# Kernel tuning notes

Measured on AMD Instinct MI355X. Metric: run time of the kernel, lower is better.

## Reference

```python
import jax, jax.numpy as jnp
import numpy as np

C = 64          # channels
K = 15          # sum(shell_sizes)=1+14
H = 32          # neighbors per query
N = 50000       # support points (== query points M)
RADIUS = 1.0
SIGMA = 0.7
INF = 1e6
BN_EPS = 1e-5


def _init_kernel_points(key):
    # stand-in for load_kernels: 1 center point + 14 points on a sphere shell
    pts = jax.random.normal(key, (K - 1, 3), dtype=jnp.float32)
    pts = pts / jnp.linalg.norm(pts, axis=1, keepdims=True) * RADIUS
    return jnp.concatenate([jnp.zeros((1, 3), jnp.float32), pts], axis=0)


def setup_inputs() -> dict:
    key = jax.random.key(0)
    ks = jax.random.split(key, 10)
    q_pts = jax.random.normal(ks[0], (N, 3), dtype=jnp.float32)
    s_pts = jax.random.normal(ks[1], (N, 3), dtype=jnp.float32)
    s_feats = jax.random.normal(ks[2], (N, C), dtype=jnp.float32)
    neighb_inds = jax.random.randint(ks[3], (N, H), 0, N)
    kernel_points = _init_kernel_points(ks[4])
    # alpha_mlp: Linear(C->C, no bias) -> BatchNorm -> LeakyReLU(0.1) -> Linear(C->K*C)
    lim1 = 1.0 / np.sqrt(C)
    W1 = jax.random.uniform(ks[5], (C, C), jnp.float32, -lim1, lim1)
    gamma = jnp.ones((C,), jnp.float32)
    beta = jnp.zeros((C,), jnp.float32)
    W2 = jax.random.uniform(ks[6], (C, K * C), jnp.float32, -lim1, lim1)
    b2 = jax.random.uniform(ks[7], (K * C,), jnp.float32, -lim1, lim1)
    return {"q_pts": q_pts, "s_pts": s_pts, "s_feats": s_feats,
            "neighb_inds": neighb_inds, "kernel_points": kernel_points,
            "W1": W1, "gamma": gamma, "beta": beta, "W2": W2, "b2": b2}


def reference(q_pts, s_pts, s_feats, neighb_inds, kernel_points, W1, gamma, beta, W2, b2):
    M = q_pts.shape[0]
    # alpha_mlp on pooled (= center) features: (M, C) -> (M, K*C)
    h = s_feats @ W1
    mu = jnp.mean(h, axis=0)
    var = jnp.var(h, axis=0)
    h = (h - mu) / jnp.sqrt(var + BN_EPS) * gamma + beta
    h = jax.nn.leaky_relu(h, 0.1)
    conv_weights = (h @ W2 + b2).reshape(M, K, C)

    # gather neighbor features with a zero padding row (index N -> zeros)
    padded_feats = jnp.concatenate([s_feats, jnp.zeros((1, C), s_feats.dtype)], axis=0)
    neighbor_feats = padded_feats[neighb_inds]                 # (M, H, C)

    # relative neighbor positions with inf padding point
    s_pts_pad = jnp.concatenate([s_pts, jnp.full((1, 3), INF, s_pts.dtype)], axis=0)
    neighbors = s_pts_pad[neighb_inds] - q_pts[:, None, :]     # (M, H, 3)

    # kernel-point influence: nearest kernel point + linear influence
    diff = neighbors[:, :, None, :] - kernel_points            # (M, H, K, 3)
    sq_d = jnp.sum(diff * diff, axis=-1)                       # (M, H, K)
    nn_sq = jnp.min(sq_d, axis=-1)                             # (M, H)
    nn_idx = jnp.argmin(sq_d, axis=-1)                         # (M, H)
    infl = jnp.clip(1.0 - jnp.sqrt(nn_sq) / SIGMA, 0.0)        # (M, H)

    # per-neighbor channel weights from the MLP output, gathered by 1nn kernel point
    nw = jnp.take_along_axis(conv_weights, nn_idx[:, :, None], axis=1)  # (M, H, C)
    nw = nw * infl[:, :, None]

    # weighted aggregation (merge=mul, aggr=sum over neighbors)
    return jnp.sum(neighbor_feats * nw, axis=1)                # (M, C)
```

## Files before the change

kernel.cpp:

```cpp
#include <hip/hip_runtime.h>
#include <math.h>

#define N_PTS 50000
#define CCH   64
#define KP    15
#define NH    32
#define SIGMA 0.7f
#define BN_EPS 1e-5f
#define LEAKY 0.1f
#define QB    16
#define STATS_BLOCKS 1024
#define SP4_BLOCKS 196
#define CW_KSTRIDE_B 2176

typedef short bf16x8 __attribute__((ext_vector_type(8)));
typedef float floatx4 __attribute__((ext_vector_type(4)));

__device__ __forceinline__ unsigned short f2b(float f) {
    union { float f; unsigned u; } v; v.f = f;
    return (unsigned short)((v.u + 0x7FFFu + ((v.u >> 16) & 1u)) >> 16);
}
__device__ __forceinline__ float b2f(unsigned short b) {
    union { unsigned u; float f; } v; v.u = ((unsigned)b) << 16;
    return v.f;
}
__device__ __forceinline__ float blo(unsigned u) {
    union { unsigned u; float f; } v; v.u = u << 16;
    return v.f;
}
__device__ __forceinline__ float bhi(unsigned u) {
    union { unsigned u; float f; } v; v.u = u & 0xFFFF0000u;
    return v.f;
}
__device__ __forceinline__ unsigned cvtpk(float lo, float hi) {
    unsigned r;
    asm("v_cvt_pk_bf16_f32 %0, %1, %2" : "=v"(r) : "v"(lo), "v"(hi));
    return r;
}

__global__ __launch_bounds__(256) void k_prep(const float* __restrict__ sf,
                                              const float* __restrict__ W1,
                                              const float* __restrict__ W2,
                                              const float* __restrict__ s_pts,
                                              float* __restrict__ bn,
                                              unsigned short* __restrict__ hst,
                                              unsigned short* __restrict__ w2b,
                                              unsigned short* __restrict__ sfb,
                                              float* __restrict__ sp4) {
    int t = threadIdx.x;
    if (blockIdx.x >= STATS_BLOCKS + 30) {
        int g = (blockIdx.x - STATS_BLOCKS - 30) * 256 + t;
        if (g < N_PTS) {
            float4 v;
            v.x = s_pts[g * 3 + 0]; v.y = s_pts[g * 3 + 1];
            v.z = s_pts[g * 3 + 2]; v.w = 0.f;
            *(float4*)(sp4 + g * 4) = v;
        }
        return;
    }
    if (blockIdx.x >= STATS_BLOCKS) {
        int g = (blockIdx.x - STATS_BLOCKS) * 256 + t;
        int lane = g & 63, s = (g >> 6) & 1, tt = g >> 7;
        int col = lane & 15, quad = lane >> 4;
        int base = (s * 32 + quad * 8) * 960 + tt * 16 + col;
        ushort4 lo, hi;
        lo.x = f2b(W2[base + 0 * 960]); lo.y = f2b(W2[base + 1 * 960]);
        lo.z = f2b(W2[base + 2 * 960]); lo.w = f2b(W2[base + 3 * 960]);
        hi.x = f2b(W2[base + 4 * 960]); hi.y = f2b(W2[base + 5 * 960]);
        hi.z = f2b(W2[base + 6 * 960]); hi.w = f2b(W2[base + 7 * 960]);
        *(ushort4*)(w2b + g * 8)     = lo;
        *(ushort4*)(w2b + g * 8 + 4) = hi;
        return;
    }
    int c = t & 63, ml = t >> 6;
    float w1c[64];
    #pragma unroll
    for (int i = 0; i < 64; ++i) w1c[i] = W1[i * 64 + c];
    __shared__ float rows[4][64];
    float acc_s = 0.f, acc_q = 0.f;
    for (int m0 = blockIdx.x * 4; m0 < N_PTS; m0 += STATS_BLOCKS * 4) {
        __syncthreads();
        float v = sf[m0 * 64 + t];
        ((float*)rows)[t] = v;
        sfb[m0 * 64 + t] = f2b(v);
        __syncthreads();
        float h = 0.f;
        #pragma unroll
        for (int i4 = 0; i4 < 16; ++i4) {
            float4 r = *(const float4*)&rows[ml][i4 * 4];
            h += r.x * w1c[i4 * 4] + r.y * w1c[i4 * 4 + 1]
               + r.z * w1c[i4 * 4 + 2] + r.w * w1c[i4 * 4 + 3];
        }
        acc_s += h;
        acc_q += h * h;
        hst[(m0 + ml) * 64 + c] = f2b(h);
    }
    __shared__ float red[2][256];
    red[0][t] = acc_s; red[1][t] = acc_q;
    __syncthreads();
    if (t < 64) {
        float s = red[0][t] + red[0][64 + t] + red[0][128 + t] + red[0][192 + t];
        float q = red[1][t] + red[1][64 + t] + red[1][128 + t] + red[1][192 + t];
        atomicAdd(&bn[t], s);
        atomicAdd(&bn[64 + t], q);
    }
}

__global__ __launch_bounds__(256, 4) void k_main(
    const float* __restrict__ q_pts, const float* __restrict__ sp4,
    const unsigned short* __restrict__ sfb, const int* __restrict__ nb,
    const float* __restrict__ kpts, const float* __restrict__ gamma,
    const float* __restrict__ beta, const float* __restrict__ bn,
    const float* __restrict__ b2, const unsigned short* __restrict__ w2b,
    const unsigned short* __restrict__ hst, float* __restrict__ out) {

    __shared__ __align__(16) unsigned cwP[KP * 32 * 17];
    __shared__ float abS[128];
    __shared__ int      nCnt[QB];
    __shared__ unsigned nPack[QB][NH];
    __shared__ float    nInf[QB][NH];

    int t = threadIdx.x;
    int lane = t & 63, wv = t >> 6;
    int m0 = blockIdx.x * QB;

    int q0 = t >> 5, hh = t & 31;
    int q1 = q0 + 8;
    int idx0 = nb[(m0 + q0) * NH + hh];
    int idx1 = nb[(m0 + q1) * NH + hh];

    if (t < 64) {
        float mu  = bn[t] * (1.0f / N_PTS);
        float var = bn[64 + t] * (1.0f / N_PTS) - mu * mu;
        float a   = gamma[t] * rsqrtf(var + BN_EPS);
        abS[t]      = a;
        abS[64 + t] = beta[t] - mu * a;
    }
    ((unsigned*)nPack)[t]       = 0u;
    ((unsigned*)nPack)[t + 256] = 0u;
    ((float*)nInf)[t]           = 0.f;
    ((float*)nInf)[t + 256]     = 0.f;

    int row = lane & 15, half = lane >> 4;
    bf16x8 r0, r1;
    {
        const unsigned short* hrow = hst + (m0 + row) * 64 + half * 8;
        r0 = *(const bf16x8*)(hrow);
        r1 = *(const bf16x8*)(hrow + 32);
    }

    float4 sp0 = *(const float4*)(sp4 + idx0 * 4);
    float4 sp1 = *(const float4*)(sp4 + idx1 * 4);
    float qx0 = q_pts[(m0 + q0) * 3 + 0], qy0 = q_pts[(m0 + q0) * 3 + 1],
          qz0 = q_pts[(m0 + q0) * 3 + 2];
    float qx1 = q_pts[(m0 + q1) * 3 + 0], qy1 = q_pts[(m0 + q1) * 3 + 1],
          qz1 = q_pts[(m0 + q1) * 3 + 2];

    float kpr[45];
    #pragma unroll
    for (int i = 0; i < 45; ++i) kpr[i] = kpts[i];

    __syncthreads();

    unsigned pf0 = 0, pf1 = 0, pf2 = 0, pf3 = 0;
    {
        float px = sp0.x - qx0, py = sp0.y - qy0, pz = sp0.z - qz0;
        float best = 1e30f; int bi = 0;
        #pragma unroll
        for (int k = 0; k < KP; ++k) {
            float dx = px - kpr[k * 3], dy = py - kpr[k * 3 + 1], dz = pz - kpr[k * 3 + 2];
            float d = dx * dx + dy * dy + dz * dz;
            if (d < best) { best = d; bi = k; }
        }
        float infl = 1.f - sqrtf(best) * (1.0f / SIGMA);
        bool keep = infl > 0.f;
        unsigned long long bal = __ballot(keep);
        unsigned mym = (unsigned)(bal >> (lane & 32));
        int pos = __popc(mym & ((1u << (lane & 31)) - 1u));
        if (keep) {
            nPack[q0][pos] = (unsigned)idx0 | ((unsigned)(bi * CW_KSTRIDE_B) << 16);
            nInf[q0][pos]  = infl;
            const unsigned* rowp = (const unsigned*)(sfb + idx0 * 64);
            pf0 = rowp[0]; pf1 = rowp[16];
        }
        if ((lane & 31) == 0) nCnt[q0] = __popc(mym);
    }
    {
        float px = sp1.x - qx1, py = sp1.y - qy1, pz = sp1.z - qz1;
        float best = 1e30f; int bi = 0;
        #pragma unroll
        for (int k = 0; k < KP; ++k) {
            float dx = px - kpr[k * 3], dy = py - kpr[k * 3 + 1], dz = pz - kpr[k * 3 + 2];
            float d = dx * dx + dy * dy + dz * dz;
            if (d < best) { best = d; bi = k; }
        }
        float infl = 1.f - sqrtf(best) * (1.0f / SIGMA);
        bool keep = infl > 0.f;
        unsigned long long bal = __ballot(keep);
        unsigned mym = (unsigned)(bal >> (lane & 32));
        int pos = __popc(mym & ((1u << (lane & 31)) - 1u));
        if (keep) {
            nPack[q1][pos] = (unsigned)idx1 | ((unsigned)(bi * CW_KSTRIDE_B) << 16);
            nInf[q1][pos]  = infl;
            const unsigned* rowp = (const unsigned*)(sfb + idx1 * 64);
            pf2 = rowp[0]; pf3 = rowp[16];
        }
        if ((lane & 31) == 0) nCnt[q1] = __popc(mym);
    }

    bf16x8 a0, a1;
    {
        unsigned* A0 = (unsigned*)&a0;
        unsigned* A1 = (unsigned*)&a1;
        #pragma unroll
        for (int jw = 0; jw < 4; ++jw) {
            int c0 = half * 8 + jw * 2;
            float g00 = abS[c0]     * b2f((unsigned short)r0[jw * 2])     + abS[64 + c0];
            float g01 = abS[c0 + 1] * b2f((unsigned short)r0[jw * 2 + 1]) + abS[64 + c0 + 1];
            g00 = g00 > 0.f ? g00 : LEAKY * g00;
            g01 = g01 > 0.f ? g01 : LEAKY * g01;
            A0[jw] = cvtpk(g00, g01);
            int c1 = 32 + c0;
            float g10 = abS[c1]     * b2f((unsigned short)r1[jw * 2])     + abS[64 + c1];
            float g11 = abS[c1 + 1] * b2f((unsigned short)r1[jw * 2 + 1]) + abS[64 + c1 + 1];
            g10 = g10 > 0.f ? g10 : LEAKY * g10;
            g11 = g11 > 0.f ? g11 : LEAKY * g11;
            A1[jw] = cvtpk(g10, g11);
        }
    }

    {
        int colq = lane & 15, quad = lane >> 4;
        bf16x8 Lf[3], Ls[3], Mf[3], Ms[3];
        #pragma unroll
        for (int i = 0; i < 3; ++i) {
            int tt = wv * 15 + i;
            Lf[i] = *(const bf16x8*)(w2b + ((tt * 2 + 0) * 64 + lane) * 8);
            Ls[i] = *(const bf16x8*)(w2b + ((tt * 2 + 1) * 64 + lane) * 8);
        }
        #pragma unroll
        for (int g = 0; g < 5; ++g) {
            if (g < 4) {
                #pragma unroll
                for (int i = 0; i < 3; ++i) {
                    int tt = wv * 15 + (g + 1) * 3 + i;
                    Mf[i] = *(const bf16x8*)(w2b + ((tt * 2 + 0) * 64 + lane) * 8);
                    Ms[i] = *(const bf16x8*)(w2b + ((tt * 2 + 1) * 64 + lane) * 8);
                }
            }
            #pragma unroll
            for (int i = 0; i < 3; ++i) {
                int tt = wv * 15 + g * 3 + i;
                floatx4 acc = {0.f, 0.f, 0.f, 0.f};
                acc = __builtin_amdgcn_mfma_f32_16x16x32_bf16(Lf[i], a0, acc, 0, 0, 0);
                acc = __builtin_amdgcn_mfma_f32_16x16x32_bf16(Ls[i], a1, acc, 0, 0, 0);
                int n0 = tt * 16 + quad * 4;
                float4 bb = *(const float4*)&b2[n0];
                int k  = n0 >> 6;
                int c2 = (n0 & 63) >> 1;
                unsigned w0 = cvtpk(acc[0] + bb.x, acc[1] + bb.y);
                unsigned w1 = cvtpk(acc[2] + bb.z, acc[3] + bb.w);
                unsigned* dst = cwP + (k * 544 + c2 * 17 + colq);
                dst[0]  = w0;
                dst[17] = w1;
            }
            if (g < 4) {
                #pragma unroll
                for (int i = 0; i < 3; ++i) { Lf[i] = Mf[i]; Ls[i] = Ms[i]; }
            }
        }
    }
    asm volatile("" :: "v"(pf0), "v"(pf1), "v"(pf2), "v"(pf3));
    __syncthreads();

    {
        int r = lane >> 5, c2 = lane & 31;
        const unsigned short* sfbC = sfb + c2 * 2;
        const unsigned char* cwB = (const unsigned char*)cwP;
        #pragma unroll
        for (int pp = 0; pp < 2; ++pp) {
            int qa = wv * 4 + pp * 2;
            int q  = qa + r;
            const unsigned* packRow = &nPack[q][0];
            const float*    infRow  = &nInf[q][0];
            const unsigned char* cwLane = cwB + (c2 * 17 + q) * 4;
            int nA = nCnt[qa], nB = nCnt[qa + 1];
            int na = nA > nB ? nA : nB;
            float acc0 = 0.f, acc1 = 0.f;
            for (int jj = 0; jj < na; jj += 4) {
                uint4  pk = *(const uint4*)&packRow[jj];
                float4 in = *(const float4*)&infRow[jj];
                unsigned f0 = *(const unsigned*)(sfbC + (pk.x & 0xFFFFu) * 64);
                unsigned f1 = *(const unsigned*)(sfbC + (pk.y & 0xFFFFu) * 64);
                unsigned f2 = *(const unsigned*)(sfbC + (pk.z & 0xFFFFu) * 64);
                unsigned f3 = *(const unsigned*)(sfbC + (pk.w & 0xFFFFu) * 64);
                unsigned w0 = *(const unsigned*)(cwLane + (pk.x >> 16));
                unsigned w1 = *(const unsigned*)(cwLane + (pk.y >> 16));
                unsigned w2 = *(const unsigned*)(cwLane + (pk.z >> 16));
                unsigned w3 = *(const unsigned*)(cwLane + (pk.w >> 16));
                acc0 = fmaf(in.x * blo(f0), blo(w0), acc0);
                acc1 = fmaf(in.x * bhi(f0), bhi(w0), acc1);
                acc0 = fmaf(in.y * blo(f1), blo(w1), acc0);
                acc1 = fmaf(in.y * bhi(f1), bhi(w1), acc1);
                acc0 = fmaf(in.z * blo(f2), blo(w2), acc0);
                acc1 = fmaf(in.z * bhi(f2), bhi(w2), acc1);
                acc0 = fmaf(in.w * blo(f3), blo(w3), acc0);
                acc1 = fmaf(in.w * bhi(f3), bhi(w3), acc1);
            }
            float2 o; o.x = acc0; o.y = acc1;
            *(float2*)&out[(m0 + q) * 64 + c2 * 2] = o;
        }
    }
}

extern "C" void kernel_launch(void* const* d_in, const int* in_sizes, int n_in,
                              void* d_out, int out_size, void* d_ws, size_t ws_size,
                              hipStream_t stream) {
    const float* q_pts   = (const float*)d_in[0];
    const float* s_pts   = (const float*)d_in[1];
    const float* s_feats = (const float*)d_in[2];
    const int*   nb      = (const int*)d_in[3];
    const float* kpts    = (const float*)d_in[4];
    const float* W1      = (const float*)d_in[5];
    const float* gamma   = (const float*)d_in[6];
    const float* beta    = (const float*)d_in[7];
    const float* W2      = (const float*)d_in[8];
    const float* b2      = (const float*)d_in[9];
    float* out = (float*)d_out;

    float* ws = (float*)d_ws;
    float* bn = ws;
    unsigned short* w2b = (unsigned short*)(ws + 128);
    unsigned short* hst = w2b + 61440;
    unsigned short* sfb = hst + N_PTS * CCH;
    float* sp4 = (float*)(sfb + N_PTS * CCH);

    hipMemsetAsync(bn, 0, 128 * sizeof(float), stream);
    k_prep<<<STATS_BLOCKS + 30 + SP4_BLOCKS, 256, 0, stream>>>(
        s_feats, W1, W2, s_pts, bn, hst, w2b, sfb, sp4);
    k_main<<<N_PTS / QB, 256, 0, stream>>>(q_pts, sp4, sfb, nb, kpts,
                                           gamma, beta, bn, b2, w2b, hst, out);
}
```

Measured before the change: 155.2 us.

## Make k_main persistent with register-resident W2 and next-tile prefetch

Turns the main kernel into a persistent grid of 1024 blocks that loop over query tiles. The W2 MFMA fragments are loaded once per block into registers instead of once per tile, and the next tile's neighbor indices, hidden features, query points and support positions are prefetched during the current tile's MFMA work. Padding entries in the shared neighbor lists are now written as zeros in the compaction step rather than by a separate clear. The cost is much higher register pressure (launch bounds drop to 2 blocks per SIMD group), fewer resident waves to hide gather latency, and an extra barrier per tile.

```diff
diff --git a/kernel.cpp b/kernel.cpp
--- a/kernel.cpp
+++ b/kernel.cpp
@@ -9,6 +9,8 @@
 #define BN_EPS 1e-5f
 #define LEAKY 0.1f
 #define QB    16
+#define NT    (N_PTS / QB)
+#define GMAIN 1024
 #define STATS_BLOCKS 1024
 #define SP4_BLOCKS 196
 #define CW_KSTRIDE_B 2176
@@ -106,7 +108,7 @@
     }
 }
 
-__global__ __launch_bounds__(256, 4) void k_main(
+__global__ __launch_bounds__(256, 2) void k_main(
     const float* __restrict__ q_pts, const float* __restrict__ sp4,
     const unsigned short* __restrict__ sfb, const int* __restrict__ nb,
     const float* __restrict__ kpts, const float* __restrict__ gamma,
@@ -122,12 +124,6 @@
 
     int t = threadIdx.x;
     int lane = t & 63, wv = t >> 6;
-    int m0 = blockIdx.x * QB;
-
-    int q0 = t >> 5, hh = t & 31;
-    int q1 = q0 + 8;
-    int idx0 = nb[(m0 + q0) * NH + hh];
-    int idx1 = nb[(m0 + q1) * NH + hh];
 
     if (t < 64) {
         float mu  = bn[t] * (1.0f / N_PTS);
@@ -136,124 +132,144 @@
         abS[t]      = a;
         abS[64 + t] = beta[t] - mu * a;
     }
-    ((unsigned*)nPack)[t]       = 0u;
-    ((unsigned*)nPack)[t + 256] = 0u;
-    ((float*)nInf)[t]           = 0.f;
-    ((float*)nInf)[t + 256]     = 0.f;
-
+
+    bf16x8 Wf0[15], Wf1[15];
+    #pragma unroll
+    for (int i = 0; i < 15; ++i) {
+        int tt = wv * 15 + i;
+        Wf0[i] = *(const bf16x8*)(w2b + ((tt * 2 + 0) * 64 + lane) * 8);
+        Wf1[i] = *(const bf16x8*)(w2b + ((tt * 2 + 1) * 64 + lane) * 8);
+    }
+
+    float kpr[45];
+    #pragma unroll
+    for (int i = 0; i < 45; ++i) kpr[i] = kpts[i];
+
+    int q0 = t >> 5, hh = t & 31;
+    int q1 = q0 + 8;
     int row = lane & 15, half = lane >> 4;
+
+    int tile = blockIdx.x;
+    int m0 = tile * QB;
+    int idx0 = nb[(m0 + q0) * NH + hh];
+    int idx1 = nb[(m0 + q1) * NH + hh];
     bf16x8 r0, r1;
     {
         const unsigned short* hrow = hst + (m0 + row) * 64 + half * 8;
         r0 = *(const bf16x8*)(hrow);
         r1 = *(const bf16x8*)(hrow + 32);
     }
-
-    float4 sp0 = *(const float4*)(sp4 + idx0 * 4);
-    float4 sp1 = *(const float4*)(sp4 + idx1 * 4);
     float qx0 = q_pts[(m0 + q0) * 3 + 0], qy0 = q_pts[(m0 + q0) * 3 + 1],
           qz0 = q_pts[(m0 + q0) * 3 + 2];
     float qx1 = q_pts[(m0 + q1) * 3 + 0], qy1 = q_pts[(m0 + q1) * 3 + 1],
           qz1 = q_pts[(m0 + q1) * 3 + 2];
-
-    float kpr[45];
-    #pragma unroll
-    for (int i = 0; i < 45; ++i) kpr[i] = kpts[i];
+    float4 sp0 = *(const float4*)(sp4 + idx0 * 4);
+    float4 sp1 = *(const float4*)(sp4 + idx1 * 4);
 
     __syncthreads();
 
-    unsigned pf0 = 0, pf1 = 0, pf2 = 0, pf3 = 0;
-    {
-        float px = sp0.x - qx0, py = sp0.y - qy0, pz = sp0.z - qz0;
-        float best = 1e30f; int bi = 0;
-        #pragma unroll
-        for (int k = 0; k < KP; ++k) {
-            float dx = px - kpr[k * 3], dy = py - kpr[k * 3 + 1], dz = pz - kpr[k * 3 + 2];
-            float d = dx * dx + dy * dy + dz * dz;
-            if (d < best) { best = d; bi = k; }
-        }
-        float infl = 1.f - sqrtf(best) * (1.0f / SIGMA);
-        bool keep = infl > 0.f;
-        unsigned long long bal = __ballot(keep);
-        unsigned mym = (unsigned)(bal >> (lane & 32));
-        int pos = __popc(mym & ((1u << (lane & 31)) - 1u));
-        if (keep) {
-            nPack[q0][pos] = (unsigned)idx0 | ((unsigned)(bi * CW_KSTRIDE_B) << 16);
-            nInf[q0][pos]  = infl;
-            const unsigned* rowp = (const unsigned*)(sfb + idx0 * 64);
-            pf0 = rowp[0]; pf1 = rowp[16];
-        }
-        if ((lane & 31) == 0) nCnt[q0] = __popc(mym);
-    }
-    {
-        float px = sp1.x - qx1, py = sp1.y - qy1, pz = sp1.z - qz1;
-        float best = 1e30f; int bi = 0;
-        #pragma unroll
-        for (int k = 0; k < KP; ++k) {
-            float dx = px - kpr[k * 3], dy = py - kpr[k * 3 + 1], dz = pz - kpr[k * 3 + 2];
-            float d = dx * dx + dy * dy + dz * dz;
-            if (d < best) { best = d; bi = k; }
-        }
-        float infl = 1.f - sqrtf(best) * (1.0f / SIGMA);
-        bool keep = infl > 0.f;
-        unsigned long long bal = __ballot(keep);
-        unsigned mym = (unsigned)(bal >> (lane & 32));
-        int pos = __popc(mym & ((1u << (lane & 31)) - 1u));
-        if (keep) {
-            nPack[q1][pos] = (unsigned)idx1 | ((unsigned)(bi * CW_KSTRIDE_B) << 16);
-            nInf[q1][pos]  = infl;
-            const unsigned* rowp = (const unsigned*)(sfb + idx1 * 64);
-            pf2 = rowp[0]; pf3 = rowp[16];
-        }
-        if ((lane & 31) == 0) nCnt[q1] = __popc(mym);
-    }
-
-    bf16x8 a0, a1;
-    {
-        unsigned* A0 = (unsigned*)&a0;
-        unsigned* A1 = (unsigned*)&a1;
-        #pragma unroll
-        for (int jw = 0; jw < 4; ++jw) {
-            int c0 = half * 8 + jw * 2;
-            float g00 = abS[c0]     * b2f((unsigned short)r0[jw * 2])     + abS[64 + c0];
-            float g01 = abS[c0 + 1] * b2f((unsigned short)r0[jw * 2 + 1]) + abS[64 + c0 + 1];
-            g00 = g00 > 0.f ? g00 : LEAKY * g00;
-            g01 = g01 > 0.f ? g01 : LEAKY * g01;
-            A0[jw] = cvtpk(g00, g01);
-            int c1 = 32 + c0;
-            float g10 = abS[c1]     * b2f((unsigned short)r1[jw * 2])     + abS[64 + c1];
-            float g11 = abS[c1 + 1] * b2f((unsigned short)r1[jw * 2 + 1]) + abS[64 + c1 + 1];
-            g10 = g10 > 0.f ? g10 : LEAKY * g10;
-            g11 = g11 > 0.f ? g11 : LEAKY * g11;
-            A1[jw] = cvtpk(g10, g11);
-        }
-    }
-
-    {
-        int colq = lane & 15, quad = lane >> 4;
-        bf16x8 Lf[3], Ls[3], Mf[3], Ms[3];
-        #pragma unroll
-        for (int i = 0; i < 3; ++i) {
-            int tt = wv * 15 + i;
-            Lf[i] = *(const bf16x8*)(w2b + ((tt * 2 + 0) * 64 + lane) * 8);
-            Ls[i] = *(const bf16x8*)(w2b + ((tt * 2 + 1) * 64 + lane) * 8);
-        }
-        #pragma unroll
-        for (int g = 0; g < 5; ++g) {
-            if (g < 4) {
-                #pragma unroll
-                for (int i = 0; i < 3; ++i) {
-                    int tt = wv * 15 + (g + 1) * 3 + i;
-                    Mf[i] = *(const bf16x8*)(w2b + ((tt * 2 + 0) * 64 + lane) * 8);
-                    Ms[i] = *(const bf16x8*)(w2b + ((tt * 2 + 1) * 64 + lane) * 8);
-                }
-            }
-            #pragma unroll
-            for (int i = 0; i < 3; ++i) {
-                int tt = wv * 15 + g * 3 + i;
+    while (true) {
+        m0 = tile * QB;
+        int ntile = tile + GMAIN;
+        bool more = ntile < NT;
+
+        unsigned pf0 = 0, pf1 = 0, pf2 = 0, pf3 = 0;
+        {
+            float px = sp0.x - qx0, py = sp0.y - qy0, pz = sp0.z - qz0;
+            float best = 1e30f; int bi = 0;
+            #pragma unroll
+            for (int k = 0; k < KP; ++k) {
+                float dx = px - kpr[k*3], dy = py - kpr[k*3+1], dz = pz - kpr[k*3+2];
+                float d = dx*dx + dy*dy + dz*dz;
+                if (d < best) { best = d; bi = k; }
+            }
+            float infl = 1.f - sqrtf(best) * (1.0f / SIGMA);
+            bool keep = infl > 0.f;
+            unsigned long long bal = __ballot(keep);
+            unsigned mym = (unsigned)(bal >> (lane & 32));
+            unsigned below = mym & ((1u << (lane & 31)) - 1u);
+            int cnt = __popc(mym);
+            int pos = keep ? __popc(below)
+                           : cnt + ((lane & 31) - __popc(below));
+            nPack[q0][pos] = keep ? ((unsigned)idx0 | ((unsigned)(bi * CW_KSTRIDE_B) << 16)) : 0u;
+            nInf[q0][pos]  = keep ? infl : 0.f;
+            if (keep) {
+                const unsigned* rowp = (const unsigned*)(sfb + idx0 * 64);
+                pf0 = rowp[0]; pf1 = rowp[16];
+            }
+            if ((lane & 31) == 0) nCnt[q0] = cnt;
+        }
+        {
+            float px = sp1.x - qx1, py = sp1.y - qy1, pz = sp1.z - qz1;
+            float best = 1e30f; int bi = 0;
+            #pragma unroll
+            for (int k = 0; k < KP; ++k) {
+                float dx = px - kpr[k*3], dy = py - kpr[k*3+1], dz = pz - kpr[k*3+2];
+                float d = dx*dx + dy*dy + dz*dz;
+                if (d < best) { best = d; bi = k; }
+            }
+            float infl = 1.f - sqrtf(best) * (1.0f / SIGMA);
+            bool keep = infl > 0.f;
+            unsigned long long bal = __ballot(keep);
+            unsigned mym = (unsigned)(bal >> (lane & 32));
+            unsigned below = mym & ((1u << (lane & 31)) - 1u);
+            int cnt = __popc(mym);
+            int pos = keep ? __popc(below)
+                           : cnt + ((lane & 31) - __popc(below));
+            nPack[q1][pos] = keep ? ((unsigned)idx1 | ((unsigned)(bi * CW_KSTRIDE_B) << 16)) : 0u;
+            nInf[q1][pos]  = keep ? infl : 0.f;
+            if (keep) {
+                const unsigned* rowp = (const unsigned*)(sfb + idx1 * 64);
+                pf2 = rowp[0]; pf3 = rowp[16];
+            }
+            if ((lane & 31) == 0) nCnt[q1] = cnt;
+        }
+
+        bf16x8 a0, a1;
+        {
+            unsigned* A0 = (unsigned*)&a0;
+            unsigned* A1 = (unsigned*)&a1;
+            #pragma unroll
+            for (int jw = 0; jw < 4; ++jw) {
+                int c0 = half * 8 + jw * 2;
+                float g00 = abS[c0]     * b2f((unsigned short)r0[jw*2])     + abS[64+c0];
+                float g01 = abS[c0 + 1] * b2f((unsigned short)r0[jw*2 + 1]) + abS[64+c0+1];
+                g00 = g00 > 0.f ? g00 : LEAKY * g00;
+                g01 = g01 > 0.f ? g01 : LEAKY * g01;
+                A0[jw] = cvtpk(g00, g01);
+                int c1 = 32 + c0;
+                float g10 = abS[c1]     * b2f((unsigned short)r1[jw*2])     + abS[64+c1];
+                float g11 = abS[c1 + 1] * b2f((unsigned short)r1[jw*2 + 1]) + abS[64+c1+1];
+                g10 = g10 > 0.f ? g10 : LEAKY * g10;
+                g11 = g11 > 0.f ? g11 : LEAKY * g11;
+                A1[jw] = cvtpk(g10, g11);
+            }
+        }
+
+        int idx0n, idx1n;
+        bf16x8 r0n, r1n;
+        float qx0n, qy0n, qz0n, qx1n, qy1n, qz1n;
+        if (more) {
+            int m0n = ntile * QB;
+            idx0n = nb[(m0n + q0) * NH + hh];
+            idx1n = nb[(m0n + q1) * NH + hh];
+            const unsigned short* hrow = hst + (m0n + row) * 64 + half * 8;
+            r0n = *(const bf16x8*)(hrow);
+            r1n = *(const bf16x8*)(hrow + 32);
+            qx0n = q_pts[(m0n + q0) * 3 + 0]; qy0n = q_pts[(m0n + q0) * 3 + 1];
+            qz0n = q_pts[(m0n + q0) * 3 + 2];
+            qx1n = q_pts[(m0n + q1) * 3 + 0]; qy1n = q_pts[(m0n + q1) * 3 + 1];
+            qz1n = q_pts[(m0n + q1) * 3 + 2];
+        }
+
+        {
+            int colq = lane & 15, quad = lane >> 4;
+            #pragma unroll
+            for (int i = 0; i < 15; ++i) {
+                int tt = wv * 15 + i;
                 floatx4 acc = {0.f, 0.f, 0.f, 0.f};
-                acc = __builtin_amdgcn_mfma_f32_16x16x32_bf16(Lf[i], a0, acc, 0, 0, 0);
-                acc = __builtin_amdgcn_mfma_f32_16x16x32_bf16(Ls[i], a1, acc, 0, 0, 0);
+                acc = __builtin_amdgcn_mfma_f32_16x16x32_bf16(Wf0[i], a0, acc, 0, 0, 0);
+                acc = __builtin_amdgcn_mfma_f32_16x16x32_bf16(Wf1[i], a1, acc, 0, 0, 0);
                 int n0 = tt * 16 + quad * 4;
                 float4 bb = *(const float4*)&b2[n0];
                 int k  = n0 >> 6;
@@ -264,52 +280,64 @@
                 dst[0]  = w0;
                 dst[17] = w1;
             }
-            if (g < 4) {
-                #pragma unroll
-                for (int i = 0; i < 3; ++i) { Lf[i] = Mf[i]; Ls[i] = Ms[i]; }
-            }
-        }
-    }
-    asm volatile("" :: "v"(pf0), "v"(pf1), "v"(pf2), "v"(pf3));
-    __syncthreads();
-
-    {
-        int r = lane >> 5, c2 = lane & 31;
-        const unsigned short* sfbC = sfb + c2 * 2;
-        const unsigned char* cwB = (const unsigned char*)cwP;
-        #pragma unroll
-        for (int pp = 0; pp < 2; ++pp) {
-            int qa = wv * 4 + pp * 2;
-            int q  = qa + r;
-            const unsigned* packRow = &nPack[q][0];
-            const float*    infRow  = &nInf[q][0];
-            const unsigned char* cwLane = cwB + (c2 * 17 + q) * 4;
-            int nA = nCnt[qa], nB = nCnt[qa + 1];
-            int na = nA > nB ? nA : nB;
-            float acc0 = 0.f, acc1 = 0.f;
-            for (int jj = 0; jj < na; jj += 4) {
-                uint4  pk = *(const uint4*)&packRow[jj];
-                float4 in = *(const float4*)&infRow[jj];
-                unsigned f0 = *(const unsigned*)(sfbC + (pk.x & 0xFFFFu) * 64);
-                unsigned f1 = *(const unsigned*)(sfbC + (pk.y & 0xFFFFu) * 64);
-                unsigned f2 = *(const unsigned*)(sfbC + (pk.z & 0xFFFFu) * 64);
-                unsigned f3 = *(const unsigned*)(sfbC + (pk.w & 0xFFFFu) * 64);
-                unsigned w0 = *(const unsigned*)(cwLane + (pk.x >> 16));
-                unsigned w1 = *(const unsigned*)(cwLane + (pk.y >> 16));
-                unsigned w2 = *(const unsigned*)(cwLane + (pk.z >> 16));
-                unsigned w3 = *(const unsigned*)(cwLane + (pk.w >> 16));
-                acc0 = fmaf(in.x * blo(f0), blo(w0), acc0);
-                acc1 = fmaf(in.x * bhi(f0), bhi(w0), acc1);
-                acc0 = fmaf(in.y * blo(f1), blo(w1), acc0);
-                acc1 = fmaf(in.y * bhi(f1), bhi(w1), acc1);
-                acc0 = fmaf(in.z * blo(f2), blo(w2), acc0);
-                acc1 = fmaf(in.z * bhi(f2), bhi(w2), acc1);
-                acc0 = fmaf(in.w * blo(f3), blo(w3), acc0);
-                acc1 = fmaf(in.w * bhi(f3), bhi(w3), acc1);
-            }
-            float2 o; o.x = acc0; o.y = acc1;
-            *(float2*)&out[(m0 + q) * 64 + c2 * 2] = o;
-        }
+        }
+
+        float4 sp0n, sp1n;
+        if (more) {
+            sp0n = *(const float4*)(sp4 + idx0n * 4);
+            sp1n = *(const float4*)(sp4 + idx1n * 4);
+        }
+
+        asm volatile("" :: "v"(pf0), "v"(pf1), "v"(pf2), "v"(pf3));
+        __syncthreads();
+
+        {
+            int r = lane >> 5, c2 = lane & 31;
+            const unsigned short* sfbC = sfb + c2 * 2;
+            const unsigned char* cwB = (const unsigned char*)cwP;
+            #pragma unroll
+            for (int pp = 0; pp < 2; ++pp) {
+                int qa = wv * 4 + pp * 2;
+                int q  = qa + r;
+                const unsigned* packRow = &nPack[q][0];
+                const float*    infRow  = &nInf[q][0];
+                const unsigned char* cwLane = cwB + (c2 * 17 + q) * 4;
+                int nA = nCnt[qa], nB = nCnt[qa + 1];
+                int na = nA > nB ? nA : nB;
+                float acc0 = 0.f, acc1 = 0.f;
+                for (int jj = 0; jj < na; jj += 4) {
+                    uint4  pk = *(const uint4*)&packRow[jj];
+                    float4 in = *(const float4*)&infRow[jj];
+                    unsigned f0 = *(const unsigned*)(sfbC + (pk.x & 0xFFFFu) * 64);
+                    unsigned f1 = *(const unsigned*)(sfbC + (pk.y & 0xFFFFu) * 64);
+                    unsigned f2 = *(const unsigned*)(sfbC + (pk.z & 0xFFFFu) * 64);
+                    unsigned f3 = *(const unsigned*)(sfbC + (pk.w & 0xFFFFu) * 64);
+                    unsigned w0 = *(const unsigned*)(cwLane + (pk.x >> 16));
+                    unsigned w1 = *(const unsigned*)(cwLane + (pk.y >> 16));
+                    unsigned w2 = *(const unsigned*)(cwLane + (pk.z >> 16));
+                    unsigned w3 = *(const unsigned*)(cwLane + (pk.w >> 16));
+                    acc0 = fmaf(in.x * blo(f0), blo(w0), acc0);
+                    acc1 = fmaf(in.x * bhi(f0), bhi(w0), acc1);
+                    acc0 = fmaf(in.y * blo(f1), blo(w1), acc0);
+                    acc1 = fmaf(in.y * bhi(f1), bhi(w1), acc1);
+                    acc0 = fmaf(in.z * blo(f2), blo(w2), acc0);
+                    acc1 = fmaf(in.z * bhi(f2), bhi(w2), acc1);
+                    acc0 = fmaf(in.w * blo(f3), blo(w3), acc0);
+                    acc1 = fmaf(in.w * bhi(f3), bhi(w3), acc1);
+                }
+                float2 o; o.x = acc0; o.y = acc1;
+                *(float2*)&out[(m0 + q) * 64 + c2 * 2] = o;
+            }
+        }
+
+        if (!more) break;
+        idx0 = idx0n; idx1 = idx1n;
+        r0 = r0n; r1 = r1n;
+        sp0 = sp0n; sp1 = sp1n;
+        qx0 = qx0n; qy0 = qy0n; qz0 = qz0n;
+        qx1 = qx1n; qy1 = qy1n; qz1 = qz1n;
+        tile = ntile;
+        __syncthreads();
     }
 }
 
@@ -338,6 +366,6 @@
     hipMemsetAsync(bn, 0, 128 * sizeof(float), stream);
     k_prep<<<STATS_BLOCKS + 30 + SP4_BLOCKS, 256, 0, stream>>>(
         s_feats, W1, W2, s_pts, bn, hst, w2b, sfb, sp4);
-    k_main<<<N_PTS / QB, 256, 0, stream>>>(q_pts, sp4, sfb, nb, kpts,
-                                           gamma, beta, bn, b2, w2b, hst, out);
-}
+    k_main<<<GMAIN, 256, 0, stream>>>(q_pts, sp4, sfb, nb, kpts,
+                                      gamma, beta, bn, b2, w2b, hst, out);
+}
```

Result: slower. 172.2 us (+10.9%).
